# Kernel tuning notes

Hardware: AMD Instinct MI355X
Metric: run time of the kernel (lower is better)

The kernel has to match this reference:

```python
import jax, jax.numpy as jnp
import numpy as np

N = 16384      # total points
B = 8          # point clouds in batch
PER = N // B   # points per cloud (batch ids sorted in blocks)
M = 4096       # sampled centers (ratio 0.25, strided sampler -> batch-aligned)
K = 64         # max_num_neighbors
R = 0.25       # ball-query radius
C_IN = 128
HID = 256
C_OUT = 256


def setup_inputs() -> dict:
    key = jax.random.key(0)
    k1, k2, k3, k4, k5 = jax.random.split(key, 5)
    x = jax.random.normal(k1, (N, C_IN), dtype=jnp.float32)
    pos = jax.random.uniform(k2, (N, 3), dtype=jnp.float32)  # unit cube
    batch = jnp.repeat(jnp.arange(B, dtype=jnp.int32), PER)  # sorted block batch ids
    lframes = jax.random.normal(k3, (N, 3, 3), dtype=jnp.float32)
    W1 = jax.random.normal(k4, (2 * C_IN + 3, HID), dtype=jnp.float32) * 0.05
    b1 = jnp.zeros((HID,), dtype=jnp.float32)
    W2 = jax.random.normal(k5, (HID, C_OUT), dtype=jnp.float32) * 0.05
    b2 = jnp.zeros((C_OUT,), dtype=jnp.float32)
    return {"x": x, "pos": pos, "batch": batch, "lframes": lframes,
            "W1": W1, "b1": b1, "W2": W2, "b2": b2}


def _ball_query(pos, batch, idx):
    """radius(pos, pos[idx], R, batch, batch[idx], max_num_neighbors=K).
    Returns fixed-size neighbor indices [M, K] + validity mask [M, K]."""
    pos_c = pos[idx]                                  # [M, 3]
    # squared distances via gemm trick (avoid [M, N, 3] broadcast)
    d2 = ((pos_c ** 2).sum(-1)[:, None]
          + (pos ** 2).sum(-1)[None, :]
          - 2.0 * pos_c @ pos.T)                      # [M, N]
    valid = (d2 <= R * R) & (batch[idx][:, None] == batch[None, :])
    score = jnp.where(valid, -d2, -jnp.inf)
    vals, nbr = jax.lax.top_k(score, K)               # K nearest within ball
    return nbr, jnp.isfinite(vals)


def reference(x, pos, batch, lframes, W1, b1, W2, b2):
    # center sampler: strided subsample (batch-aligned since batch is block-sorted)
    idx = jnp.arange(0, N, N // M)                    # [M]
    nbr, vmask = _ball_query(pos, batch, idx)         # [M, K]

    pos_dst = pos[idx]                                # [M, 3]
    x_dst = x[idx]                                    # [M, C_IN]
    lframes_dst = lframes[idx]                        # [M, 3, 3]

    # EdgeConv: per-edge message MLP([x_src, x_dst, lframe_dst @ (pos_src - pos_dst)])
    rel = pos[nbr] - pos_dst[:, None, :]              # [M, K, 3]
    rel_loc = jnp.einsum('mij,mkj->mki', lframes_dst, rel)  # rotate into dst frame
    feats = jnp.concatenate([
        x[nbr],                                        # [M, K, C_IN]
        jnp.broadcast_to(x_dst[:, None, :], (M, K, C_IN)),
        rel_loc,
    ], axis=-1)                                        # [M, K, 2*C_IN+3]

    h = jax.nn.relu(feats @ W1 + b1)                   # [M, K, HID]
    msg = h @ W2 + b2                                  # [M, K, C_OUT]

    # masked max aggregation over valid neighbors
    msg = jnp.where(vmask[..., None], msg, -jnp.inf)
    out = msg.max(axis=1)                              # [M, C_OUT]
    out = jnp.where(jnp.isfinite(out), out, 0.0)
    return out, pos_dst, batch[idx], lframes_dst
```

## Files before the change

kernel.cpp:

```cpp
#include <hip/hip_runtime.h>
#include <hip/hip_bf16.h>

#define N_PTS 16384
#define PER   2048
#define M_CTR 4096
#define KNB   64
#define C_IN  128
#define HID   256
#define C_OUT 256

typedef unsigned short u16;
typedef unsigned int u32;
typedef __attribute__((ext_vector_type(8))) short s8v;
typedef __attribute__((ext_vector_type(4))) float f4v;
typedef __attribute__((ext_vector_type(4))) unsigned int u4v;

static __device__ __forceinline__ u16 f2bf(float f) {
    union { float f; unsigned int i; } v; v.f = f;
    unsigned int r = v.i + 0x7FFFu + ((v.i >> 16) & 1u);
    return (u16)(r >> 16);
}

__global__ __launch_bounds__(256) void ballq_kernel(
        const float* __restrict__ pos, int* __restrict__ nbr, int* __restrict__ cnt,
        const float* __restrict__ W1, const float* __restrict__ W2,
        u16* __restrict__ W1aT, u16* __restrict__ W1bT, u16* __restrict__ W2T) {
    __shared__ float cd2[1024];
    __shared__ int   cidx[1024];
    __shared__ int   s_n;
    int m = blockIdx.x, tid = threadIdx.x;

    if (m < 256) {
        int gid = m * 256 + tid;
        int cc = gid >> 8, k = gid & 255;
        W2T[gid] = f2bf(W2[k * 256 + cc]);
        if (gid < 32768) {
            int c1 = gid >> 7, k1 = gid & 127;
            W1aT[gid] = f2bf(W1[k1 * 256 + c1]);
            W1bT[gid] = f2bf(W1[(k1 + 128) * 256 + c1]);
        }
    }

    int c = m * 4;
    int base = (m >> 9) << 11;
    int ln = tid & 63;
    if (tid == 0) s_n = 0;
    __syncthreads();
    float cx = pos[c * 3 + 0], cy = pos[c * 3 + 1], cz = pos[c * 3 + 2];
    float A = __fadd_rn(__fadd_rn(__fmul_rn(cx, cx), __fmul_rn(cy, cy)), __fmul_rn(cz, cz));
    float c2x = __fmul_rn(2.0f, cx);
    float c2y = __fmul_rn(2.0f, cy);
    float c2z = __fmul_rn(2.0f, cz);
    for (int s = 0; s < 8; ++s) {
        int j = base + tid + (s << 8);
        float px = pos[j * 3 + 0], py = pos[j * 3 + 1], pz = pos[j * 3 + 2];
        float B = __fadd_rn(__fadd_rn(__fmul_rn(px, px), __fmul_rn(py, py)), __fmul_rn(pz, pz));
        float C = __fmaf_rn(c2z, pz, __fmaf_rn(c2y, py, __fmul_rn(c2x, px)));
        float d2 = __fsub_rn(__fadd_rn(A, B), C);
        bool hit = (d2 <= 0.0625f);
        unsigned long long mk = __ballot(hit);
        int nb = __popcll(mk & ((1ull << ln) - 1ull));
        int tot = __popcll(mk);
        int bidx = 0;
        if (ln == 0 && tot) bidx = atomicAdd(&s_n, tot);
        bidx = __shfl(bidx, 0, 64);
        if (hit) {
            int a = bidx + nb;
            if (a < 1024) { cd2[a] = d2; cidx[a] = j; }
        }
    }
    __syncthreads();
    int V = s_n < 1024 ? s_n : 1024;
    if (V <= KNB) {
        if (tid < KNB) nbr[m * KNB + tid] = (tid < V) ? cidx[tid] : c;
        if (tid == 0) cnt[m] = V;
    } else {
        for (int e = tid; e < V; e += 256) {
            float de = cd2[e]; int ie = cidx[e];
            int rank = 0;
            for (int q = 0; q < V; ++q) {
                float dq = cd2[q];
                rank += (dq < de) || (dq == de && cidx[q] < ie);
            }
            if (rank < KNB) nbr[m * KNB + rank] = cidx[e];
        }
        if (tid == 0) cnt[m] = KNB;
    }
}

__global__ __launch_bounds__(256) void gemm_xw_kernel(
        const float* __restrict__ x, const u16* __restrict__ W1aT, const u16* __restrict__ W1bT,
        const float* __restrict__ b1, u16* __restrict__ u_out, float* __restrict__ v_out) {
    __shared__ u16 x_lds[64 * 136];
    int blk = blockIdx.x, tid = threadIdx.x;
    int mode = blk >= 256 ? 1 : 0;
    int bb = mode ? blk - 256 : blk;
    const u16* WT = mode ? W1bT : W1aT;
    {
        int r = tid >> 2, q = tid & 3;
        int xrow = bb * 64 + r;
        if (mode) xrow *= 4;
        const float* xp = x + xrow * C_IN + q * 32;
        u16* dst = x_lds + r * 136 + q * 32;
        for (int i = 0; i < 8; ++i) {
            f4v f = *(const f4v*)(xp + i * 4);
            dst[i * 4 + 0] = f2bf(f[0]);
            dst[i * 4 + 1] = f2bf(f[1]);
            dst[i * 4 + 2] = f2bf(f[2]);
            dst[i * 4 + 3] = f2bf(f[3]);
        }
    }
    __syncthreads();
    int lane = tid & 63, w = tid >> 6;
    int quad = lane >> 4, l16 = lane & 15;
    int cb = w * 64;
    f4v acc[4][4] = {};
    for (int k0 = 0; k0 < 128; k0 += 32) {
        s8v a[4], b[4];
        for (int rt = 0; rt < 4; ++rt)
            a[rt] = *(const s8v*)&x_lds[(rt * 16 + l16) * 136 + k0 + quad * 8];
        for (int ct = 0; ct < 4; ++ct)
            b[ct] = *(const s8v*)(WT + (cb + ct * 16 + l16) * 128 + k0 + quad * 8);
        for (int rt = 0; rt < 4; ++rt)
            for (int ct = 0; ct < 4; ++ct)
                acc[rt][ct] = __builtin_amdgcn_mfma_f32_16x16x32_bf16(a[rt], b[ct], acc[rt][ct], 0, 0, 0);
    }
    for (int rt = 0; rt < 4; ++rt)
        for (int ct = 0; ct < 4; ++ct)
            for (int g = 0; g < 4; ++g) {
                int row = rt * 16 + quad * 4 + g;
                int col = cb + ct * 16 + l16;
                float val = acc[rt][ct][g];
                int orow = bb * 64 + row;
                if (mode == 0) u_out[orow * 256 + col] = f2bf(val);
                else           v_out[orow * 256 + col] = val + b1[col];
            }
}

__global__ __launch_bounds__(512, 2) void edge_kernel(
        const u16* __restrict__ u, const float* __restrict__ v,
        const u16* __restrict__ W2T, const float* __restrict__ W1,
        const float* __restrict__ b2, const float* __restrict__ pos,
        const float* __restrict__ lframes, const int* __restrict__ batch,
        const int* __restrict__ nbrg, const int* __restrict__ cnt,
        float* __restrict__ out0, float* __restrict__ out_pos,
        float* __restrict__ out_batch, float* __restrict__ out_lf) {
    __shared__ u16   h_lds[2][128 * 264];
    __shared__ float v_lds[2][2][256];
    __shared__ float w1c_lds[768];
    __shared__ f4v   relc_lds[2][2][64];
    __shared__ u16   nbr_lds[2][2][64];

    int blk = blockIdx.x, tid = threadIdx.x;
    int m0 = ((blk & 7) << 9) | ((blk >> 3) << 3);

    int lane = tid & 63, w = tid >> 6;
    int quad = lane >> 4, l16 = lane & 15;
    int cb = (w & 3) * 64;
    int rbase = (w >> 2) * 64;
    int gsel = w >> 2;

    s8v bfrag[6][4];
    #pragma unroll
    for (int k0 = 0; k0 < 6; ++k0)
        #pragma unroll
        for (int ct = 0; ct < 4; ++ct)
            bfrag[k0][ct] = *(const s8v*)(W2T + (cb + ct * 16 + l16) * 256 + k0 * 32 + quad * 8);

    for (int i = tid; i < 768; i += 512) w1c_lds[i] = W1[65536 + i];
    if (tid < 128) {
        int g = tid >> 6, t = tid & 63;
        int mm = m0 + g, cc = mm * 4;
        int j = nbrg[mm * KNB + t];
        nbr_lds[0][g][t] = (u16)j;
        float rx = pos[j * 3 + 0] - pos[cc * 3 + 0];
        float ry = pos[j * 3 + 1] - pos[cc * 3 + 1];
        float rz = pos[j * 3 + 2] - pos[cc * 3 + 2];
        const float* lf = lframes + cc * 9;
        f4v r;
        r[0] = lf[0] * rx + lf[1] * ry + lf[2] * rz;
        r[1] = lf[3] * rx + lf[4] * ry + lf[5] * rz;
        r[2] = lf[6] * rx + lf[7] * ry + lf[8] * rz;
        r[3] = 0.0f;
        relc_lds[0][g][t] = r;
    }
    v_lds[0][tid >> 8][tid & 255] = v[(m0 + (tid >> 8)) * 256 + (tid & 255)];
    if (tid >= 256 && tid < 384) {
        int g = (tid - 256) >> 4, t = tid & 15;
        int mm = m0 + g, cc = mm * 4;
        if (t < 3)            out_pos[mm * 3 + t] = pos[cc * 3 + t];
        else if (t == 3)      out_batch[mm] = (float)batch[cc];
        else if (t < 13)      out_lf[mm * 9 + (t - 4)] = lframes[cc * 9 + (t - 4)];
    }

    int co = (tid & 31) * 8;
    int rs = tid >> 5;
    int cv_cur = cnt[m0 + gsel];
    __syncthreads();

    int cv_next = 0;
    for (int p = 0; p < 4; ++p) {
        int pb = p & 1;
        #pragma unroll
        for (int g = 0; g < 2; ++g) {
            f4v vq0 = *(const f4v*)&v_lds[pb][g][co];
            f4v vq1 = *(const f4v*)&v_lds[pb][g][co + 4];
            f4v wa0 = *(const f4v*)&w1c_lds[co],       wa1 = *(const f4v*)&w1c_lds[co + 4];
            f4v wb0 = *(const f4v*)&w1c_lds[256 + co], wb1 = *(const f4v*)&w1c_lds[256 + co + 4];
            f4v wc0 = *(const f4v*)&w1c_lds[512 + co], wc1 = *(const f4v*)&w1c_lds[512 + co + 4];
            #pragma unroll
            for (int i2 = 0; i2 < 4; ++i2) {
                int rl = rs + i2 * 16;
                int row = g * 64 + rl;
                int j = (int)nbr_lds[pb][g][rl];
                u4v uu = *(const u4v*)(u + j * 256 + co);
                f4v r = relc_lds[pb][g][rl];
                float p8[8];
                #pragma unroll
                for (int e = 0; e < 8; ++e) {
                    u32 bits = (e & 1) ? (uu[e >> 1] & 0xFFFF0000u) : (uu[e >> 1] << 16);
                    float va = (e < 4) ? vq0[e] : vq1[e - 4];
                    float a0 = (e < 4) ? wa0[e] : wa1[e - 4];
                    float b0 = (e < 4) ? wb0[e] : wb1[e - 4];
                    float c0 = (e < 4) ? wc0[e] : wc1[e - 4];
                    float pre = fmaf(r[0], a0, fmaf(r[1], b0, fmaf(r[2], c0,
                                  va + __uint_as_float(bits))));
                    p8[e] = fmaxf(pre, 0.0f);
                }
                u4v pk;
                #pragma unroll
                for (int d = 0; d < 4; ++d)
                    pk[d] = __builtin_amdgcn_perm(__float_as_uint(p8[2 * d + 1]),
                                                  __float_as_uint(p8[2 * d]), 0x07060302u);
                *(u4v*)&h_lds[pb][row * 264 + co] = pk;
            }
        }
        if (p < 3) {
            int nb = pb ^ 1;
            int mbase = m0 + (p + 1) * 2;
            cv_next = cnt[mbase + gsel];
            if (tid < 128) {
                int g = tid >> 6, t = tid & 63;
                int mm = mbase + g, cc = mm * 4;
                int j = nbrg[mm * KNB + t];
                nbr_lds[nb][g][t] = (u16)j;
                float rx = pos[j * 3 + 0] - pos[cc * 3 + 0];
                float ry = pos[j * 3 + 1] - pos[cc * 3 + 1];
                float rz = pos[j * 3 + 2] - pos[cc * 3 + 2];
                const float* lf = lframes + cc * 9;
                f4v r;
                r[0] = lf[0] * rx + lf[1] * ry + lf[2] * rz;
                r[1] = lf[3] * rx + lf[4] * ry + lf[5] * rz;
                r[2] = lf[6] * rx + lf[7] * ry + lf[8] * rz;
                r[3] = 0.0f;
                relc_lds[nb][g][t] = r;
            }
            v_lds[nb][tid >> 8][tid & 255] = v[(mbase + (tid >> 8)) * 256 + (tid & 255)];
        }
        __syncthreads();

        s8v bs[2][4];
        #pragma unroll
        for (int kk = 0; kk < 2; ++kk)
            #pragma unroll
            for (int ct = 0; ct < 4; ++ct)
                bs[kk][ct] = *(const s8v*)(W2T + (cb + ct * 16 + l16) * 256 + (6 + kk) * 32 + quad * 8);
        f4v acc[4][4] = {};
        #pragma unroll
        for (int k0 = 0; k0 < 6; ++k0) {
            s8v a[4];
            #pragma unroll
            for (int rt = 0; rt < 4; ++rt)
                a[rt] = *(const s8v*)&h_lds[pb][(rbase + rt * 16 + l16) * 264 + k0 * 32 + quad * 8];
            #pragma unroll
            for (int rt = 0; rt < 4; ++rt)
                #pragma unroll
                for (int ct = 0; ct < 4; ++ct)
                    acc[rt][ct] = __builtin_amdgcn_mfma_f32_16x16x32_bf16(a[rt], bfrag[k0][ct], acc[rt][ct], 0, 0, 0);
        }
        #pragma unroll
        for (int kk = 0; kk < 2; ++kk) {
            int k0 = 6 + kk;
            s8v a[4];
            #pragma unroll
            for (int rt = 0; rt < 4; ++rt)
                a[rt] = *(const s8v*)&h_lds[pb][(rbase + rt * 16 + l16) * 264 + k0 * 32 + quad * 8];
            #pragma unroll
            for (int rt = 0; rt < 4; ++rt)
                #pragma unroll
                for (int ct = 0; ct < 4; ++ct)
                    acc[rt][ct] = __builtin_amdgcn_mfma_f32_16x16x32_bf16(a[rt], bs[kk][ct], acc[rt][ct], 0, 0, 0);
        }
        int mout = m0 + p * 2 + gsel;
        #pragma unroll
        for (int ct = 0; ct < 4; ++ct) {
            float mx = -__builtin_inff();
            #pragma unroll
            for (int rt = 0; rt < 4; ++rt)
                #pragma unroll
                for (int g = 0; g < 4; ++g) {
                    int row = rt * 16 + quad * 4 + g;
                    float val = acc[rt][ct][g];
                    if (row < cv_cur) mx = fmaxf(mx, val);
                }
            mx = fmaxf(mx, __shfl_xor(mx, 16, 64));
            mx = fmaxf(mx, __shfl_xor(mx, 32, 64));
            if (lane < 16)
                out0[mout * 256 + cb + ct * 16 + l16] = mx + b2[cb + ct * 16 + l16];
        }
        cv_cur = cv_next;
    }
}

extern "C" void kernel_launch(void* const* d_in, const int* in_sizes, int n_in,
                              void* d_out, int out_size, void* d_ws, size_t ws_size,
                              hipStream_t stream) {
    const float* x       = (const float*)d_in[0];
    const float* pos     = (const float*)d_in[1];
    const int*   batch   = (const int*)d_in[2];
    const float* lframes = (const float*)d_in[3];
    const float* W1      = (const float*)d_in[4];
    const float* b1      = (const float*)d_in[5];
    const float* W2      = (const float*)d_in[6];
    const float* b2      = (const float*)d_in[7];

    float* out       = (float*)d_out;
    float* out_pos   = out + M_CTR * 256;
    float* out_batch = out_pos + M_CTR * 3;
    float* out_lf    = out_batch + M_CTR;

    char* ws = (char*)d_ws;
    u16*   u_ws = (u16*)(ws);
    float* v_ws = (float*)(ws + 8388608);
    u16*   W1aT = (u16*)(ws + 12582912);
    u16*   W1bT = (u16*)(ws + 12648448);
    u16*   W2T  = (u16*)(ws + 12713984);
    int*   nbr  = (int*)(ws + 12845056);
    int*   cntp = (int*)(ws + 13893632);

    hipLaunchKernelGGL(ballq_kernel, dim3(M_CTR), dim3(256), 0, stream,
                       pos, nbr, cntp, W1, W2, W1aT, W1bT, W2T);
    hipLaunchKernelGGL(gemm_xw_kernel, dim3(320), dim3(256), 0, stream,
                       x, W1aT, W1bT, b1, u_ws, v_ws);
    hipLaunchKernelGGL(edge_kernel, dim3(512), dim3(512), 0, stream,
                       u_ws, v_ws, W2T, W1, b2, pos, lframes, batch, nbr, cntp,
                       out, out_pos, out_batch, out_lf);
}
```

Measured before the change: 172.1 us.

## Merge ball query and node GEMM kernels; raise edge kernel occupancy

The ball-query and x@W1 GEMM kernels are merged into one launch whose blocks branch by index and share an LDS arena. The GEMM now reads and converts fp32 W1 directly instead of using a pre-transposed bf16 copy. In the edge kernel, the W2 fragments are no longer held in registers and h_lds is single-buffered with an extra barrier, so launch bounds can ask for 4 blocks per CU. The aim is to cut launch gaps and raise occupancy, at the cost of reloading W2 from global memory each pass, losing the double buffer overlap, and doing uncoalesced strided W1 loads in the GEMM.

```diff
diff --git a/kernel.cpp b/kernel.cpp
--- a/kernel.cpp
+++ b/kernel.cpp
@@ -21,123 +21,135 @@
     return (u16)(r >> 16);
 }
 
-__global__ __launch_bounds__(256) void ballq_kernel(
+__global__ __launch_bounds__(256) void work_kernel(
         const float* __restrict__ pos, int* __restrict__ nbr, int* __restrict__ cnt,
         const float* __restrict__ W1, const float* __restrict__ W2,
-        u16* __restrict__ W1aT, u16* __restrict__ W1bT, u16* __restrict__ W2T) {
-    __shared__ float cd2[1024];
-    __shared__ int   cidx[1024];
-    __shared__ int   s_n;
-    int m = blockIdx.x, tid = threadIdx.x;
-
-    if (m < 256) {
-        int gid = m * 256 + tid;
-        int cc = gid >> 8, k = gid & 255;
-        W2T[gid] = f2bf(W2[k * 256 + cc]);
-        if (gid < 32768) {
-            int c1 = gid >> 7, k1 = gid & 127;
-            W1aT[gid] = f2bf(W1[k1 * 256 + c1]);
-            W1bT[gid] = f2bf(W1[(k1 + 128) * 256 + c1]);
-        }
-    }
-
-    int c = m * 4;
-    int base = (m >> 9) << 11;
-    int ln = tid & 63;
-    if (tid == 0) s_n = 0;
-    __syncthreads();
-    float cx = pos[c * 3 + 0], cy = pos[c * 3 + 1], cz = pos[c * 3 + 2];
-    float A = __fadd_rn(__fadd_rn(__fmul_rn(cx, cx), __fmul_rn(cy, cy)), __fmul_rn(cz, cz));
-    float c2x = __fmul_rn(2.0f, cx);
-    float c2y = __fmul_rn(2.0f, cy);
-    float c2z = __fmul_rn(2.0f, cz);
-    for (int s = 0; s < 8; ++s) {
-        int j = base + tid + (s << 8);
-        float px = pos[j * 3 + 0], py = pos[j * 3 + 1], pz = pos[j * 3 + 2];
-        float B = __fadd_rn(__fadd_rn(__fmul_rn(px, px), __fmul_rn(py, py)), __fmul_rn(pz, pz));
-        float C = __fmaf_rn(c2z, pz, __fmaf_rn(c2y, py, __fmul_rn(c2x, px)));
-        float d2 = __fsub_rn(__fadd_rn(A, B), C);
-        bool hit = (d2 <= 0.0625f);
-        unsigned long long mk = __ballot(hit);
-        int nb = __popcll(mk & ((1ull << ln) - 1ull));
-        int tot = __popcll(mk);
-        int bidx = 0;
-        if (ln == 0 && tot) bidx = atomicAdd(&s_n, tot);
-        bidx = __shfl(bidx, 0, 64);
-        if (hit) {
-            int a = bidx + nb;
-            if (a < 1024) { cd2[a] = d2; cidx[a] = j; }
-        }
-    }
-    __syncthreads();
-    int V = s_n < 1024 ? s_n : 1024;
-    if (V <= KNB) {
-        if (tid < KNB) nbr[m * KNB + tid] = (tid < V) ? cidx[tid] : c;
-        if (tid == 0) cnt[m] = V;
+        u16* __restrict__ W2T,
+        const float* __restrict__ x, const float* __restrict__ b1,
+        u16* __restrict__ u_out, float* __restrict__ v_out) {
+    __shared__ char arena[64 * 136 * 2];
+    int blk = blockIdx.x, tid = threadIdx.x;
+
+    if (blk < M_CTR) {
+        float* cd2 = (float*)arena;
+        int*   cidx = (int*)(arena + 4096);
+        __shared__ int s_n;
+        int m = blk;
+
+        if (m < 256) {
+            int gid = m * 256 + tid;
+            int cc = gid >> 8, k = gid & 255;
+            W2T[gid] = f2bf(W2[k * 256 + cc]);
+        }
+
+        int c = m * 4;
+        int base = (m >> 9) << 11;
+        int ln = tid & 63;
+        if (tid == 0) s_n = 0;
+        __syncthreads();
+        float cx = pos[c * 3 + 0], cy = pos[c * 3 + 1], cz = pos[c * 3 + 2];
+        float A = __fadd_rn(__fadd_rn(__fmul_rn(cx, cx), __fmul_rn(cy, cy)), __fmul_rn(cz, cz));
+        float c2x = __fmul_rn(2.0f, cx);
+        float c2y = __fmul_rn(2.0f, cy);
+        float c2z = __fmul_rn(2.0f, cz);
+        for (int s = 0; s < 8; ++s) {
+            int j = base + tid + (s << 8);
+            float px = pos[j * 3 + 0], py = pos[j * 3 + 1], pz = pos[j * 3 + 2];
+            float B = __fadd_rn(__fadd_rn(__fmul_rn(px, px), __fmul_rn(py, py)), __fmul_rn(pz, pz));
+            float C = __fmaf_rn(c2z, pz, __fmaf_rn(c2y, py, __fmul_rn(c2x, px)));
+            float d2 = __fsub_rn(__fadd_rn(A, B), C);
+            bool hit = (d2 <= 0.0625f);
+            unsigned long long mk = __ballot(hit);
+            int nb = __popcll(mk & ((1ull << ln) - 1ull));
+            int tot = __popcll(mk);
+            int bidx = 0;
+            if (ln == 0 && tot) bidx = atomicAdd(&s_n, tot);
+            bidx = __shfl(bidx, 0, 64);
+            if (hit) {
+                int a = bidx + nb;
+                if (a < 1024) { cd2[a] = d2; cidx[a] = j; }
+            }
+        }
+        __syncthreads();
+        int V = s_n < 1024 ? s_n : 1024;
+        if (V <= KNB) {
+            if (tid < KNB) nbr[m * KNB + tid] = (tid < V) ? cidx[tid] : c;
+            if (tid == 0) cnt[m] = V;
+        } else {
+            for (int e = tid; e < V; e += 256) {
+                float de = cd2[e]; int ie = cidx[e];
+                int rank = 0;
+                for (int q = 0; q < V; ++q) {
+                    float dq = cd2[q];
+                    rank += (dq < de) || (dq == de && cidx[q] < ie);
+                }
+                if (rank < KNB) nbr[m * KNB + rank] = cidx[e];
+            }
+            if (tid == 0) cnt[m] = KNB;
+        }
     } else {
-        for (int e = tid; e < V; e += 256) {
-            float de = cd2[e]; int ie = cidx[e];
-            int rank = 0;
-            for (int q = 0; q < V; ++q) {
-                float dq = cd2[q];
-                rank += (dq < de) || (dq == de && cidx[q] < ie);
-            }
-            if (rank < KNB) nbr[m * KNB + rank] = cidx[e];
-        }
-        if (tid == 0) cnt[m] = KNB;
+        u16* x_lds = (u16*)arena;
+        int blk2 = blk - M_CTR;
+        int mode = blk2 >= 256 ? 1 : 0;
+        int bb = mode ? blk2 - 256 : blk2;
+        const float* W1x = W1 + (mode ? 128 * 256 : 0);
+        {
+            int r = tid >> 2, q = tid & 3;
+            int xrow = bb * 64 + r;
+            if (mode) xrow *= 4;
+            const float* xp = x + xrow * C_IN + q * 32;
+            u16* dst = x_lds + r * 136 + q * 32;
+            for (int i = 0; i < 8; ++i) {
+                f4v f = *(const f4v*)(xp + i * 4);
+                dst[i * 4 + 0] = f2bf(f[0]);
+                dst[i * 4 + 1] = f2bf(f[1]);
+                dst[i * 4 + 2] = f2bf(f[2]);
+                dst[i * 4 + 3] = f2bf(f[3]);
+            }
+        }
+        __syncthreads();
+        int lane = tid & 63, w = tid >> 6;
+        int quad = lane >> 4, l16 = lane & 15;
+        int cb = w * 64;
+        f4v acc[4][4] = {};
+        for (int k0 = 0; k0 < 128; k0 += 32) {
+            s8v a[4], b[4];
+            #pragma unroll
+            for (int ct = 0; ct < 4; ++ct) {
+                int col = cb + ct * 16 + l16;
+                const float* wp = W1x + (k0 + quad * 8) * 256 + col;
+                union { u4v v4; s8v s8; } pk;
+                #pragma unroll
+                for (int d = 0; d < 4; ++d) {
+                    u16 lo = f2bf(wp[(2 * d) * 256]);
+                    u16 hi = f2bf(wp[(2 * d + 1) * 256]);
+                    pk.v4[d] = ((u32)hi << 16) | lo;
+                }
+                b[ct] = pk.s8;
+            }
+            #pragma unroll
+            for (int rt = 0; rt < 4; ++rt)
+                a[rt] = *(const s8v*)&x_lds[(rt * 16 + l16) * 136 + k0 + quad * 8];
+            #pragma unroll
+            for (int rt = 0; rt < 4; ++rt)
+                #pragma unroll
+                for (int ct = 0; ct < 4; ++ct)
+                    acc[rt][ct] = __builtin_amdgcn_mfma_f32_16x16x32_bf16(a[rt], b[ct], acc[rt][ct], 0, 0, 0);
+        }
+        for (int rt = 0; rt < 4; ++rt)
+            for (int ct = 0; ct < 4; ++ct)
+                for (int g = 0; g < 4; ++g) {
+                    int row = rt * 16 + quad * 4 + g;
+                    int col = cb + ct * 16 + l16;
+                    float val = acc[rt][ct][g];
+                    int orow = bb * 64 + row;
+                    if (mode == 0) u_out[orow * 256 + col] = f2bf(val);
+                    else           v_out[orow * 256 + col] = val + b1[col];
+                }
     }
 }
 
-__global__ __launch_bounds__(256) void gemm_xw_kernel(
-        const float* __restrict__ x, const u16* __restrict__ W1aT, const u16* __restrict__ W1bT,
-        const float* __restrict__ b1, u16* __restrict__ u_out, float* __restrict__ v_out) {
-    __shared__ u16 x_lds[64 * 136];
-    int blk = blockIdx.x, tid = threadIdx.x;
-    int mode = blk >= 256 ? 1 : 0;
-    int bb = mode ? blk - 256 : blk;
-    const u16* WT = mode ? W1bT : W1aT;
-    {
-        int r = tid >> 2, q = tid & 3;
-        int xrow = bb * 64 + r;
-        if (mode) xrow *= 4;
-        const float* xp = x + xrow * C_IN + q * 32;
-        u16* dst = x_lds + r * 136 + q * 32;
-        for (int i = 0; i < 8; ++i) {
-            f4v f = *(const f4v*)(xp + i * 4);
-            dst[i * 4 + 0] = f2bf(f[0]);
-            dst[i * 4 + 1] = f2bf(f[1]);
-            dst[i * 4 + 2] = f2bf(f[2]);
-            dst[i * 4 + 3] = f2bf(f[3]);
-        }
-    }
-    __syncthreads();
-    int lane = tid & 63, w = tid >> 6;
-    int quad = lane >> 4, l16 = lane & 15;
-    int cb = w * 64;
-    f4v acc[4][4] = {};
-    for (int k0 = 0; k0 < 128; k0 += 32) {
-        s8v a[4], b[4];
-        for (int rt = 0; rt < 4; ++rt)
-            a[rt] = *(const s8v*)&x_lds[(rt * 16 + l16) * 136 + k0 + quad * 8];
-        for (int ct = 0; ct < 4; ++ct)
-            b[ct] = *(const s8v*)(WT + (cb + ct * 16 + l16) * 128 + k0 + quad * 8);
-        for (int rt = 0; rt < 4; ++rt)
-            for (int ct = 0; ct < 4; ++ct)
-                acc[rt][ct] = __builtin_amdgcn_mfma_f32_16x16x32_bf16(a[rt], b[ct], acc[rt][ct], 0, 0, 0);
-    }
-    for (int rt = 0; rt < 4; ++rt)
-        for (int ct = 0; ct < 4; ++ct)
-            for (int g = 0; g < 4; ++g) {
-                int row = rt * 16 + quad * 4 + g;
-                int col = cb + ct * 16 + l16;
-                float val = acc[rt][ct][g];
-                int orow = bb * 64 + row;
-                if (mode == 0) u_out[orow * 256 + col] = f2bf(val);
-                else           v_out[orow * 256 + col] = val + b1[col];
-            }
-}
-
-__global__ __launch_bounds__(512, 2) void edge_kernel(
+__global__ __launch_bounds__(512, 4) void edge_kernel(
         const u16* __restrict__ u, const float* __restrict__ v,
         const u16* __restrict__ W2T, const float* __restrict__ W1,
         const float* __restrict__ b2, const float* __restrict__ pos,
@@ -145,7 +157,7 @@
         const int* __restrict__ nbrg, const int* __restrict__ cnt,
         float* __restrict__ out0, float* __restrict__ out_pos,
         float* __restrict__ out_batch, float* __restrict__ out_lf) {
-    __shared__ u16   h_lds[2][128 * 264];
+    __shared__ u16   h_lds[128 * 264];
     __shared__ float v_lds[2][2][256];
     __shared__ float w1c_lds[768];
     __shared__ f4v   relc_lds[2][2][64];
@@ -159,13 +171,6 @@
     int cb = (w & 3) * 64;
     int rbase = (w >> 2) * 64;
     int gsel = w >> 2;
-
-    s8v bfrag[6][4];
-    #pragma unroll
-    for (int k0 = 0; k0 < 6; ++k0)
-        #pragma unroll
-        for (int ct = 0; ct < 4; ++ct)
-            bfrag[k0][ct] = *(const s8v*)(W2T + (cb + ct * 16 + l16) * 256 + k0 * 32 + quad * 8);
 
     for (int i = tid; i < 768; i += 512) w1c_lds[i] = W1[65536 + i];
     if (tid < 128) {
@@ -232,7 +237,7 @@
                 for (int d = 0; d < 4; ++d)
                     pk[d] = __builtin_amdgcn_perm(__float_as_uint(p8[2 * d + 1]),
                                                   __float_as_uint(p8[2 * d]), 0x07060302u);
-                *(u4v*)&h_lds[pb][row * 264 + co] = pk;
+                *(u4v*)&h_lds[row * 264 + co] = pk;
             }
         }
         if (p < 3) {
@@ -259,37 +264,20 @@
         }
         __syncthreads();
 
-        s8v bs[2][4];
-        #pragma unroll
-        for (int kk = 0; kk < 2; ++kk)
+        f4v acc[4][4] = {};
+        for (int k0 = 0; k0 < 256; k0 += 32) {
+            s8v a[4], b[4];
+            #pragma unroll
+            for (int rt = 0; rt < 4; ++rt)
+                a[rt] = *(const s8v*)&h_lds[(rbase + rt * 16 + l16) * 264 + k0 + quad * 8];
             #pragma unroll
             for (int ct = 0; ct < 4; ++ct)
-                bs[kk][ct] = *(const s8v*)(W2T + (cb + ct * 16 + l16) * 256 + (6 + kk) * 32 + quad * 8);
-        f4v acc[4][4] = {};
-        #pragma unroll
-        for (int k0 = 0; k0 < 6; ++k0) {
-            s8v a[4];
-            #pragma unroll
-            for (int rt = 0; rt < 4; ++rt)
-                a[rt] = *(const s8v*)&h_lds[pb][(rbase + rt * 16 + l16) * 264 + k0 * 32 + quad * 8];
+                b[ct] = *(const s8v*)(W2T + (cb + ct * 16 + l16) * 256 + k0 + quad * 8);
             #pragma unroll
             for (int rt = 0; rt < 4; ++rt)
                 #pragma unroll
                 for (int ct = 0; ct < 4; ++ct)
-                    acc[rt][ct] = __builtin_amdgcn_mfma_f32_16x16x32_bf16(a[rt], bfrag[k0][ct], acc[rt][ct], 0, 0, 0);
-        }
-        #pragma unroll
-        for (int kk = 0; kk < 2; ++kk) {
-            int k0 = 6 + kk;
-            s8v a[4];
-            #pragma unroll
-            for (int rt = 0; rt < 4; ++rt)
-                a[rt] = *(const s8v*)&h_lds[pb][(rbase + rt * 16 + l16) * 264 + k0 * 32 + quad * 8];
-            #pragma unroll
-            for (int rt = 0; rt < 4; ++rt)
-                #pragma unroll
-                for (int ct = 0; ct < 4; ++ct)
-                    acc[rt][ct] = __builtin_amdgcn_mfma_f32_16x16x32_bf16(a[rt], bs[kk][ct], acc[rt][ct], 0, 0, 0);
+                    acc[rt][ct] = __builtin_amdgcn_mfma_f32_16x16x32_bf16(a[rt], b[ct], acc[rt][ct], 0, 0, 0);
         }
         int mout = m0 + p * 2 + gsel;
         #pragma unroll
@@ -309,6 +297,7 @@
                 out0[mout * 256 + cb + ct * 16 + l16] = mx + b2[cb + ct * 16 + l16];
         }
         cv_cur = cv_next;
+        __syncthreads();
     }
 }
 
@@ -332,16 +321,12 @@
     char* ws = (char*)d_ws;
     u16*   u_ws = (u16*)(ws);
     float* v_ws = (float*)(ws + 8388608);
-    u16*   W1aT = (u16*)(ws + 12582912);
-    u16*   W1bT = (u16*)(ws + 12648448);
     u16*   W2T  = (u16*)(ws + 12713984);
     int*   nbr  = (int*)(ws + 12845056);
     int*   cntp = (int*)(ws + 13893632);
 
-    hipLaunchKernelGGL(ballq_kernel, dim3(M_CTR), dim3(256), 0, stream,
-                       pos, nbr, cntp, W1, W2, W1aT, W1bT, W2T);
-    hipLaunchKernelGGL(gemm_xw_kernel, dim3(320), dim3(256), 0, stream,
-                       x, W1aT, W1bT, b1, u_ws, v_ws);
+    hipLaunchKernelGGL(work_kernel, dim3(M_CTR + 320), dim3(256), 0, stream,
+                       pos, nbr, cntp, W1, W2, W2T, x, b1, u_ws, v_ws);
     hipLaunchKernelGGL(edge_kernel, dim3(512), dim3(512), 0, stream,
                        u_ws, v_ws, W2T, W1, b2, pos, lframes, batch, nbr, cntp,
                        out, out_pos, out_batch, out_lf);
```

Measured after the change: 260.4 us. +51.3%, slower.
